# Optimization experiments

Hardware: AMD Instinct MI355X
Metric: run time of the kernel (lower is better)

The kernel has to match this reference:

```python
import jax, jax.numpy as jnp
import numpy as np

CHANNELS = 512
NUM_HEADS = 8
NUM_GROUPS = 32
EPS = 1e-5


def setup_inputs() -> dict:
    key = jax.random.key(0)
    ks = jax.random.split(key, 6)
    c = CHANNELS
    x = jax.random.normal(ks[0], (8, c, 32, 32), dtype=jnp.float32)
    norm_w = jnp.ones((c,), jnp.float32)
    norm_b = jnp.zeros((c,), jnp.float32)
    # 1x1 conv1d weights stored as [out, in]
    qkv_w = jax.random.normal(ks[1], (3 * c, c), jnp.float32) * (1.0 / np.sqrt(c))
    qkv_b = jax.random.normal(ks[2], (3 * c,), jnp.float32) * 0.02
    # proj_out is zero-initialized in the original; use small random values so the
    # residual branch is exercised numerically (init values are not part of the math).
    proj_w = jax.random.normal(ks[3], (c, c), jnp.float32) * 0.02
    proj_b = jax.random.normal(ks[4], (c,), jnp.float32) * 0.02
    return {"x": x, "norm_w": norm_w, "norm_b": norm_b,
            "qkv_w": qkv_w, "qkv_b": qkv_b, "proj_w": proj_w, "proj_b": proj_b}


def _group_norm(x, w, b):
    # x: [B, C, L]; normalize per (batch, group) over (C/G, L) in float32
    B, C, L = x.shape
    xg = x.astype(jnp.float32).reshape(B, NUM_GROUPS, (C // NUM_GROUPS) * L)
    mean = xg.mean(axis=-1, keepdims=True)
    var = xg.var(axis=-1, keepdims=True)
    xn = ((xg - mean) * jax.lax.rsqrt(var + EPS)).reshape(B, C, L)
    return (xn * w[None, :, None] + b[None, :, None]).astype(x.dtype)


def _attention_legacy(qkv, n_heads):
    # qkv: [B, 3*C, L]  (QKVAttentionLegacy: split heads after reshape)
    B, width, L = qkv.shape
    ch = width // (3 * n_heads)
    q, k, v = jnp.split(qkv.reshape(B * n_heads, 3 * ch, L), 3, axis=1)
    scale = 1.0 / np.sqrt(np.sqrt(ch))
    w = jnp.einsum('bct,bcs->bts', q * scale, k * scale)  # [B*H, L, L]
    w = jax.nn.softmax(w.astype(jnp.float32), axis=-1).astype(qkv.dtype)
    a = jnp.einsum('bts,bcs->bct', w, v)  # [B*H, ch, L]
    return a.reshape(B, n_heads * ch, L)


def reference(x, norm_w, norm_b, qkv_w, qkv_b, proj_w, proj_b):
    b, c = x.shape[0], x.shape[1]
    spatial = x.shape[2:]
    x_ = x.reshape(b, c, -1)  # [B, C, L]
    xn = _group_norm(x_, norm_w, norm_b)
    qkv = jnp.einsum('oc,bcl->bol', qkv_w, xn) + qkv_b[None, :, None]
    h = _attention_legacy(qkv, NUM_HEADS)
    h = jnp.einsum('oc,bcl->bol', proj_w, h) + proj_b[None, :, None]
    return (x_ + h).reshape(b, c, *spatial)
```

## Files before the change

kernel.cpp:

```cpp
#include <hip/hip_runtime.h>
#include <hip/hip_bf16.h>
#include <stdint.h>


#define NB 8
#define NC 512
#define NL 1024
#define NHD 8
#define ND 64

typedef __attribute__((ext_vector_type(4))) float f32x4;
typedef __attribute__((ext_vector_type(8))) short bf16x8;
typedef __attribute__((ext_vector_type(4))) short bf16x4;
typedef __attribute__((ext_vector_type(4))) unsigned short u16x4;
typedef __attribute__((ext_vector_type(8))) unsigned short u16x8;

#define MFMA16(a, b, c) __builtin_amdgcn_mfma_f32_16x16x32_bf16((a), (b), (c), 0, 0, 0)

static __device__ __forceinline__ f32x4 mfma_k16(bf16x4 a, bf16x4 b, f32x4 c) {
#if __has_builtin(__builtin_amdgcn_mfma_f32_16x16x16bf16_1k)
  return __builtin_amdgcn_mfma_f32_16x16x16bf16_1k(a, b, c, 0, 0, 0);
#else
  asm("v_mfma_f32_16x16x16_bf16 %0, %1, %2, %0" : "+v"(c) : "v"(a), "v"(b));
  return c;
#endif
}

#if __has_builtin(__builtin_amdgcn_exp2f)
#define EXP2F __builtin_amdgcn_exp2f
#else
#define EXP2F exp2f
#endif

static __device__ __forceinline__ unsigned short f2bf(float f) {
  union { float f; uint32_t u; } v; v.f = f;
  uint32_t r = v.u + 0x7fffu + ((v.u >> 16) & 1u);
  return (unsigned short)(r >> 16);
}

static __device__ __forceinline__ short f2bf_h(float f) {
  __hip_bfloat16 h = __float2bfloat16(f);
  return *reinterpret_cast<short*>(&h);
}

static __device__ __forceinline__ void gl_lds16(const unsigned short* g, unsigned short* l) {
  __builtin_amdgcn_global_load_lds(
      (const __attribute__((address_space(1))) void*)g,
      (__attribute__((address_space(3))) void*)l, 16, 0, 0);
}

__global__ __launch_bounds__(256) void k_conv_w(const float* __restrict__ qkvw,
                                                const float* __restrict__ pw,
                                                unsigned short* __restrict__ qwb,
                                                unsigned short* __restrict__ pwb) {
  int i = blockIdx.x * 256 + threadIdx.x;
  const int NQ4 = (3 * NC * NC) / 4;
  if (i < NQ4) {
    f32x4 v = ((const f32x4*)qkvw)[i];
    u16x4 o; o.x = f2bf(v.x); o.y = f2bf(v.y); o.z = f2bf(v.z); o.w = f2bf(v.w);
    ((u16x4*)qwb)[i] = o;
  } else {
    int j = i - NQ4;
    f32x4 v = ((const f32x4*)pw)[j];
    u16x4 o; o.x = f2bf(v.x); o.y = f2bf(v.y); o.z = f2bf(v.z); o.w = f2bf(v.w);
    ((u16x4*)pwb)[j] = o;
  }
}

__global__ __launch_bounds__(256) void k_gnorm(const float* __restrict__ x,
                                               const float* __restrict__ nw,
                                               const float* __restrict__ nb,
                                               unsigned short* __restrict__ xnt) {
  const int b = blockIdx.x >> 5, g = blockIdx.x & 31;
  const float* base = x + ((size_t)b * NC + g * 16) * NL;
  const int t = threadIdx.x;
  f32x4 vals[16];
  float s = 0.f, ss = 0.f;
#pragma unroll
  for (int r = 0; r < 16; ++r) {
    f32x4 v = ((const f32x4*)base)[t + 256 * r];
    vals[r] = v;
    s += v.x + v.y + v.z + v.w;
    ss += v.x * v.x + v.y * v.y + v.z * v.z + v.w * v.w;
  }
#pragma unroll
  for (int m = 1; m < 64; m <<= 1) { s += __shfl_xor(s, m, 64); ss += __shfl_xor(ss, m, 64); }
  __shared__ float red[8];
  const int w = t >> 6;
  if ((t & 63) == 0) { red[w] = s; red[4 + w] = ss; }
  __syncthreads();
  s  = red[0] + red[1] + red[2] + red[3];
  ss = red[4] + red[5] + red[6] + red[7];
  const float mean = s * (1.f / 16384.f);
  const float var  = ss * (1.f / 16384.f) - mean * mean;
  const float inv  = rsqrtf(var + 1e-5f);
  u16x8 ov[4][2];
#pragma unroll
  for (int r = 0; r < 16; ++r) {
    float wcv = nw[g * 16 + r] * inv;
    float bcv = nb[g * 16 + r] - mean * wcv;
    f32x4 v = vals[r];
    ov[0][r >> 3][r & 7] = f2bf(v.x * wcv + bcv);
    ov[1][r >> 3][r & 7] = f2bf(v.y * wcv + bcv);
    ov[2][r >> 3][r & 7] = f2bf(v.z * wcv + bcv);
    ov[3][r >> 3][r & 7] = f2bf(v.w * wcv + bcv);
  }
#pragma unroll
  for (int j = 0; j < 4; ++j) {
    size_t off = ((size_t)b * NL + 4 * t + j) * NC + g * 16;
    *(u16x8*)(xnt + off)     = ov[j][0];
    *(u16x8*)(xnt + off + 8) = ov[j][1];
  }
}

__global__ __launch_bounds__(256) void k_qkv(const unsigned short* __restrict__ xnt,
                                             const unsigned short* __restrict__ qwb,
                                             const float* __restrict__ qkvb,
                                             unsigned short* __restrict__ qt,
                                             unsigned short* __restrict__ kt,
                                             unsigned short* __restrict__ vt) {
  __shared__ __align__(16) unsigned short As[128 * 64];
  __shared__ __align__(16) unsigned short Bs[128 * 64];
  const int m0 = blockIdx.x * 128;
  const int n0 = blockIdx.y * 128;
  const int b = blockIdx.z;
  const int tid = threadIdx.x, lane = tid & 63, w = tid >> 6;
  const int wr = w >> 1, wc = w & 1;

  int soff[4];
#pragma unroll
  for (int r = 0; r < 4; ++r) {
    int c = (r * 4 + w) * 64 + lane;
    int row = c >> 3, lc = (c & 7) ^ (row & 7);
    soff[r] = row * NC + lc * 8;
  }
  const unsigned short* Ap = xnt + (size_t)b * NL * NC + (size_t)m0 * NC;
  const unsigned short* Bp = qwb + (size_t)n0 * NC;

  f32x4 acc[4][4];
#pragma unroll
  for (int mi = 0; mi < 4; ++mi)
#pragma unroll
    for (int ni = 0; ni < 4; ++ni) acc[mi][ni] = (f32x4){0.f, 0.f, 0.f, 0.f};

  for (int k0 = 0; k0 < NC; k0 += 64) {
#pragma unroll
    for (int r = 0; r < 4; ++r) gl_lds16(Ap + soff[r], &As[(r * 4 + w) * 512]);
#pragma unroll
    for (int r = 0; r < 4; ++r) gl_lds16(Bp + soff[r], &Bs[(r * 4 + w) * 512]);
    Ap += 64; Bp += 64;
    __syncthreads();
#pragma unroll
    for (int ks = 0; ks < 2; ++ks) {
      bf16x8 af[4], bfr[4];
#pragma unroll
      for (int mi = 0; mi < 4; ++mi) {
        int row = wr * 64 + mi * 16 + (lane & 15);
        int ph = ((lane >> 4) + ks * 4) ^ (row & 7);
        af[mi] = *(const bf16x8*)&As[row * 64 + ph * 8];
      }
#pragma unroll
      for (int ni = 0; ni < 4; ++ni) {
        int row = wc * 64 + ni * 16 + (lane & 15);
        int ph = ((lane >> 4) + ks * 4) ^ (row & 7);
        bfr[ni] = *(const bf16x8*)&Bs[row * 64 + ph * 8];
      }
#pragma unroll
      for (int mi = 0; mi < 4; ++mi)
#pragma unroll
        for (int ni = 0; ni < 4; ++ni)
          acc[mi][ni] = MFMA16(af[mi], bfr[ni], acc[mi][ni]);
    }
    __syncthreads();
  }
#pragma unroll
  for (int ni = 0; ni < 4; ++ni) {
    int o = n0 + wc * 64 + ni * 16 + (lane & 15);
    int head = o / 192, rem = o - head * 192;
    int type = rem >> 6, ch = rem & 63;
    float bias = qkvb[o];
#pragma unroll
    for (int mi = 0; mi < 4; ++mi) {
      int l0 = m0 + wr * 64 + mi * 16 + ((lane >> 4) << 2);
      if (type == 2) {
        u16x4 pk;
#pragma unroll
        for (int i = 0; i < 4; ++i) pk[i] = f2bf(acc[mi][ni][i] + bias);
        *(u16x4*)&vt[(((size_t)(b * NHD + head) * 256 + (l0 >> 2)) * ND + ch) * 4] = pk;
      } else {
        const float sc = (type == 0)
            ? (0.35355339059327373f * 1.4426950408889634f)
            : 0.35355339059327373f;
        unsigned short* dst =
            (type == 0 ? qt : kt) + ((size_t)(b * NHD + head) * NL + l0) * ND + ch;
#pragma unroll
        for (int i = 0; i < 4; ++i)
          dst[i * ND] = f2bf((acc[mi][ni][i] + bias) * sc);
      }
    }
  }
}

__global__ __launch_bounds__(256) void k_attn(const unsigned short* __restrict__ qt,
                                              const unsigned short* __restrict__ kt,
                                              const unsigned short* __restrict__ vt,
                                              unsigned short* __restrict__ abuf) {
  __shared__ __align__(16) unsigned short Ks[2][64 * 64];
  __shared__ __align__(16) unsigned short Vs[2][64 * 64];
  const int bid = blockIdx.x;
  const int bh = (bid & 7) * 8 + (bid >> 6);
  const int tb = (bid >> 3) & 7;
  const int tid = threadIdx.x, lane = tid & 63, w = tid >> 6;
  const int lo = lane & 15, g = lane >> 4;
  const int t0 = tb * 128 + w * 32;
  const unsigned short* qb = qt + (size_t)bh * NL * ND;

  int koff[2], voff[2];
#pragma unroll
  for (int r = 0; r < 2; ++r) {
    int c = (r * 4 + w) * 64 + lane;
    int row = c >> 3, lc = (c & 7) ^ (row & 7);
    koff[r] = row * ND + lc * 8;
    voff[r] = c * 8;
  }
  const int e0 = lo * 64 + ((g ^ (lo & 7)) * 8);
  const int e1 = lo * 64 + (((4 + g) ^ (lo & 7)) * 8);
  const int vbase = g * 256 + lo * 4;

  const unsigned short* kst = kt + (size_t)bh * NL * ND;
  const unsigned short* vst = vt + (size_t)bh * NL * ND;

  bf16x8 qf[2][2];
#pragma unroll
  for (int h = 0; h < 2; ++h)
#pragma unroll
    for (int ks = 0; ks < 2; ++ks)
      qf[h][ks] = *(const bf16x8*)&qb[(size_t)(t0 + h * 16 + lo) * ND + ks * 32 + g * 8];

  f32x4 pv[2][4];
#pragma unroll
  for (int h = 0; h < 2; ++h)
#pragma unroll
    for (int ci = 0; ci < 4; ++ci) pv[h][ci] = (f32x4){0.f, 0.f, 0.f, 0.f};
  float lsum0 = 0.f, lsum1 = 0.f;

  gl_lds16(kst + koff[0], &Ks[0][w * 512]);
  gl_lds16(kst + koff[1], &Ks[0][(4 + w) * 512]);
  gl_lds16(vst + voff[0], &Vs[0][w * 512]);
  gl_lds16(vst + voff[1], &Vs[0][(4 + w) * 512]);
  kst += 4096; vst += 4096;

#define ATTN_TILE(BUF, LAST)                                                  \
  {                                                                           \
    __syncthreads();                                                          \
    if (!(LAST)) {                                                            \
      gl_lds16(kst + koff[0], &Ks[(BUF) ^ 1][w * 512]);                       \
      gl_lds16(kst + koff[1], &Ks[(BUF) ^ 1][(4 + w) * 512]);                 \
      gl_lds16(vst + voff[0], &Vs[(BUF) ^ 1][w * 512]);                       \
      gl_lds16(vst + voff[1], &Vs[(BUF) ^ 1][(4 + w) * 512]);                 \
      kst += 4096; vst += 4096;                                               \
    }                                                                         \
    f32x4 sacc[2][4];                                                         \
    _Pragma("unroll")                                                         \
    for (int h = 0; h < 2; ++h)                                               \
      _Pragma("unroll")                                                       \
      for (int sblk = 0; sblk < 4; ++sblk)                                    \
        sacc[h][sblk] = (f32x4){0.f, 0.f, 0.f, 0.f};                          \
    __builtin_amdgcn_s_setprio(1);                                            \
    _Pragma("unroll")                                                         \
    for (int sblk = 0; sblk < 4; ++sblk) {                                    \
      bf16x8 kf = *(const bf16x8*)&Ks[BUF][sblk * 1024 + e0];                 \
      sacc[0][sblk] = MFMA16(kf, qf[0][0], sacc[0][sblk]);                    \
      sacc[1][sblk] = MFMA16(kf, qf[1][0], sacc[1][sblk]);                    \
    }                                                                         \
    _Pragma("unroll")                                                         \
    for (int sblk = 0; sblk < 4; ++sblk) {                                    \
      bf16x8 kf = *(const bf16x8*)&Ks[BUF][sblk * 1024 + e1];                 \
      sacc[0][sblk] = MFMA16(kf, qf[0][1], sacc[0][sblk]);                    \
      sacc[1][sblk] = MFMA16(kf, qf[1][1], sacc[1][sblk]);                    \
    }                                                                         \
    __builtin_amdgcn_s_setprio(0);                                            \
    _Pragma("unroll")                                                         \
    for (int sblk = 0; sblk < 4; ++sblk) {                                    \
      float a0 = EXP2F(fminf(sacc[0][sblk][0], 80.f));                        \
      float a1 = EXP2F(fminf(sacc[0][sblk][1], 80.f));                        \
      float a2 = EXP2F(fminf(sacc[0][sblk][2], 80.f));                        \
      float a3 = EXP2F(fminf(sacc[0][sblk][3], 80.f));                        \
      lsum0 += (a0 + a1) + (a2 + a3);                                         \
      bf16x4 pf0;                                                             \
      pf0[0] = f2bf_h(a0); pf0[1] = f2bf_h(a1);                               \
      pf0[2] = f2bf_h(a2); pf0[3] = f2bf_h(a3);                               \
      float b0 = EXP2F(fminf(sacc[1][sblk][0], 80.f));                        \
      float b1 = EXP2F(fminf(sacc[1][sblk][1], 80.f));                        \
      float b2 = EXP2F(fminf(sacc[1][sblk][2], 80.f));                        \
      float b3 = EXP2F(fminf(sacc[1][sblk][3], 80.f));                        \
      lsum1 += (b0 + b1) + (b2 + b3);                                         \
      bf16x4 pf1;                                                             \
      pf1[0] = f2bf_h(b0); pf1[1] = f2bf_h(b1);                               \
      pf1[2] = f2bf_h(b2); pf1[3] = f2bf_h(b3);                               \
      _Pragma("unroll")                                                       \
      for (int ci = 0; ci < 4; ++ci) {                                        \
        bf16x4 vf = *(const bf16x4*)&Vs[BUF][sblk * 1024 + ci * 64 + vbase];  \
        pv[0][ci] = mfma_k16(pf0, vf, pv[0][ci]);                             \
        pv[1][ci] = mfma_k16(pf1, vf, pv[1][ci]);                             \
      }                                                                       \
    }                                                                         \
  }

  for (int it = 0; it < 16; it += 2) {
    ATTN_TILE(0, false);
    ATTN_TILE(1, it == 14);
  }
#undef ATTN_TILE

#pragma unroll
  for (int h = 0; h < 2; ++h) {
    float l = h ? lsum1 : lsum0;
    l += __shfl_xor(l, 16);
    l += __shfl_xor(l, 32);
    float li[4];
#pragma unroll
    for (int i = 0; i < 4; ++i) li[i] = 1.0f / __shfl(l, g * 4 + i, 16);
#pragma unroll
    for (int ci = 0; ci < 4; ++ci)
#pragma unroll
      for (int i = 0; i < 4; ++i) {
        int tl = t0 + h * 16 + g * 4 + i;
        abuf[((size_t)bh * NL + tl) * ND + ci * 16 + lo] = f2bf_h(pv[h][ci][i] * li[i]);
      }
  }
}

__global__ __launch_bounds__(256) void k_proj(const unsigned short* __restrict__ abuf,
                                              const unsigned short* __restrict__ pwb,
                                              const float* __restrict__ pb,
                                              const float* __restrict__ x,
                                              float* __restrict__ out) {
  __shared__ __align__(16) unsigned short As[64 * 64];
  __shared__ __align__(16) unsigned short Bs[128 * 64];
  const int m0 = blockIdx.x * 64;
  const int n0 = blockIdx.y * 128;
  const int b = blockIdx.z;
  const int tid = threadIdx.x, lane = tid & 63, w = tid >> 6;
  const int lo = lane & 15, g = lane >> 4;

  int aoff[2], boff[4];
#pragma unroll
  for (int r = 0; r < 4; ++r) {
    int c = (r * 4 + w) * 64 + lane;
    int row = c >> 3, lc = (c & 7) ^ (row & 7);
    boff[r] = row * ND + lc * 8;
    if (r < 2) aoff[r] = row * NC + lc * 8;
  }
  const unsigned short* Ap = pwb + (size_t)m0 * NC;
  const unsigned short* Bp = abuf + ((size_t)(b * NHD) * NL + n0) * ND;

  f32x4 acc[4][2];
#pragma unroll
  for (int mi = 0; mi < 4; ++mi)
#pragma unroll
    for (int ni = 0; ni < 2; ++ni) acc[mi][ni] = (f32x4){0.f, 0.f, 0.f, 0.f};

  for (int k0 = 0; k0 < NC; k0 += 64) {
#pragma unroll
    for (int r = 0; r < 2; ++r) gl_lds16(Ap + aoff[r], &As[(r * 4 + w) * 512]);
#pragma unroll
    for (int r = 0; r < 4; ++r) gl_lds16(Bp + boff[r], &Bs[(r * 4 + w) * 512]);
    Ap += 64; Bp += (size_t)NL * ND;
    __syncthreads();
#pragma unroll
    for (int ks = 0; ks < 2; ++ks) {
      bf16x8 af[4], bfr[2];
#pragma unroll
      for (int mi = 0; mi < 4; ++mi) {
        int row = mi * 16 + lo;
        int ph = (g + ks * 4) ^ (row & 7);
        af[mi] = *(const bf16x8*)&As[row * 64 + ph * 8];
      }
#pragma unroll
      for (int ni = 0; ni < 2; ++ni) {
        int row = w * 32 + ni * 16 + lo;
        int ph = (g + ks * 4) ^ (row & 7);
        bfr[ni] = *(const bf16x8*)&Bs[row * 64 + ph * 8];
      }
#pragma unroll
      for (int mi = 0; mi < 4; ++mi)
#pragma unroll
        for (int ni = 0; ni < 2; ++ni)
          acc[mi][ni] = MFMA16(af[mi], bfr[ni], acc[mi][ni]);
    }
    __syncthreads();
  }
#pragma unroll
  for (int mi = 0; mi < 4; ++mi)
#pragma unroll
    for (int i = 0; i < 4; ++i) {
      int o = m0 + mi * 16 + g * 4 + i;
      float pbv = pb[o];
#pragma unroll
      for (int ni = 0; ni < 2; ++ni) {
        int l = n0 + w * 32 + ni * 16 + lo;
        size_t idx = ((size_t)b * NC + o) * NL + l;
        out[idx] = x[idx] + acc[mi][ni][i] + pbv;
      }
    }
}

extern "C" void kernel_launch(void* const* d_in, const int* in_sizes, int n_in,
                              void* d_out, int out_size, void* d_ws, size_t ws_size,
                              hipStream_t stream) {
  const float* x    = (const float*)d_in[0];
  const float* nw   = (const float*)d_in[1];
  const float* nb   = (const float*)d_in[2];
  const float* qkvw = (const float*)d_in[3];
  const float* qkvb = (const float*)d_in[4];
  const float* pw   = (const float*)d_in[5];
  const float* pb   = (const float*)d_in[6];
  float* out = (float*)d_out;

  char* ws = (char*)d_ws;
  unsigned short* xnt  = (unsigned short*)(ws);
  unsigned short* abuf = (unsigned short*)(ws);
  unsigned short* qwb  = (unsigned short*)(ws + 8388608);
  unsigned short* pwb  = (unsigned short*)(ws + 9961472);
  unsigned short* qt   = (unsigned short*)(ws + 10485760);
  unsigned short* kt   = (unsigned short*)(ws + 18874368);
  unsigned short* vt   = (unsigned short*)(ws + 27262976);

  k_conv_w<<<1024, 256, 0, stream>>>(qkvw, pw, qwb, pwb);
  k_gnorm<<<256, 256, 0, stream>>>(x, nw, nb, xnt);
  k_qkv<<<dim3(8, 12, 8), 256, 0, stream>>>(xnt, qwb, qkvb, qt, kt, vt);
  k_attn<<<512, 256, 0, stream>>>(qt, kt, vt, abuf);
  k_proj<<<dim3(8, 8, 8), 256, 0, stream>>>(abuf, pwb, pb, x, out);
}
```

Baseline: 92.96 us.

## Merge prep kernels, compute softmax row sums via MFMA, enlarge proj tile

Folds the weight-to-bf16 conversion and group norm into a single launch, which removes one kernel launch and its boundary. In attention, the per-row exp sums are now produced by an extra MFMA against a ones vector rather than VALU adds plus cross-lane shuffles, and the PV MFMAs are issued under raised wave priority. The projection GEMM tile grows from 64x128 to 128x128 with a 2x2 wave layout, halving the grid and giving more reuse per block. The risks are extra MFMA work and higher register pressure, and the row sums are now accumulated from bf16-rounded probabilities.

```diff
diff --git a/kernel.cpp b/kernel.cpp
--- a/kernel.cpp
+++ b/kernel.cpp
@@ -49,28 +49,29 @@
       (__attribute__((address_space(3))) void*)l, 16, 0, 0);
 }
 
-__global__ __launch_bounds__(256) void k_conv_w(const float* __restrict__ qkvw,
-                                                const float* __restrict__ pw,
-                                                unsigned short* __restrict__ qwb,
-                                                unsigned short* __restrict__ pwb) {
-  int i = blockIdx.x * 256 + threadIdx.x;
-  const int NQ4 = (3 * NC * NC) / 4;
-  if (i < NQ4) {
-    f32x4 v = ((const f32x4*)qkvw)[i];
-    u16x4 o; o.x = f2bf(v.x); o.y = f2bf(v.y); o.z = f2bf(v.z); o.w = f2bf(v.w);
-    ((u16x4*)qwb)[i] = o;
-  } else {
-    int j = i - NQ4;
-    f32x4 v = ((const f32x4*)pw)[j];
-    u16x4 o; o.x = f2bf(v.x); o.y = f2bf(v.y); o.z = f2bf(v.z); o.w = f2bf(v.w);
-    ((u16x4*)pwb)[j] = o;
-  }
-}
-
-__global__ __launch_bounds__(256) void k_gnorm(const float* __restrict__ x,
-                                               const float* __restrict__ nw,
-                                               const float* __restrict__ nb,
-                                               unsigned short* __restrict__ xnt) {
+__global__ __launch_bounds__(256) void k_pre(const float* __restrict__ x,
+                                             const float* __restrict__ nw,
+                                             const float* __restrict__ nb,
+                                             const float* __restrict__ qkvw,
+                                             const float* __restrict__ pw,
+                                             unsigned short* __restrict__ xnt,
+                                             unsigned short* __restrict__ qwb,
+                                             unsigned short* __restrict__ pwb) {
+  if (blockIdx.x >= 256) {
+    int i = (blockIdx.x - 256) * 256 + threadIdx.x;
+    const int NQ4 = (3 * NC * NC) / 4;
+    if (i < NQ4) {
+      f32x4 v = ((const f32x4*)qkvw)[i];
+      u16x4 o; o.x = f2bf(v.x); o.y = f2bf(v.y); o.z = f2bf(v.z); o.w = f2bf(v.w);
+      ((u16x4*)qwb)[i] = o;
+    } else {
+      int j = i - NQ4;
+      f32x4 v = ((const f32x4*)pw)[j];
+      u16x4 o; o.x = f2bf(v.x); o.y = f2bf(v.y); o.z = f2bf(v.z); o.w = f2bf(v.w);
+      ((u16x4*)pwb)[j] = o;
+    }
+    return;
+  }
   const int b = blockIdx.x >> 5, g = blockIdx.x & 31;
   const float* base = x + ((size_t)b * NC + g * 16) * NL;
   const int t = threadIdx.x;
@@ -237,12 +238,18 @@
     for (int ks = 0; ks < 2; ++ks)
       qf[h][ks] = *(const bf16x8*)&qb[(size_t)(t0 + h * 16 + lo) * ND + ks * 32 + g * 8];
 
+  bf16x4 vones;
+#pragma unroll
+  for (int j = 0; j < 4; ++j) vones[j] = (short)0x3F80;
+
   f32x4 pv[2][4];
 #pragma unroll
   for (int h = 0; h < 2; ++h)
 #pragma unroll
     for (int ci = 0; ci < 4; ++ci) pv[h][ci] = (f32x4){0.f, 0.f, 0.f, 0.f};
-  float lsum0 = 0.f, lsum1 = 0.f;
+  f32x4 lacc[2];
+  lacc[0] = (f32x4){0.f, 0.f, 0.f, 0.f};
+  lacc[1] = (f32x4){0.f, 0.f, 0.f, 0.f};
 
   gl_lds16(kst + koff[0], &Ks[0][w * 512]);
   gl_lds16(kst + koff[1], &Ks[0][(4 + w) * 512]);
@@ -286,7 +293,6 @@
       float a1 = EXP2F(fminf(sacc[0][sblk][1], 80.f));                        \
       float a2 = EXP2F(fminf(sacc[0][sblk][2], 80.f));                        \
       float a3 = EXP2F(fminf(sacc[0][sblk][3], 80.f));                        \
-      lsum0 += (a0 + a1) + (a2 + a3);                                         \
       bf16x4 pf0;                                                             \
       pf0[0] = f2bf_h(a0); pf0[1] = f2bf_h(a1);                               \
       pf0[2] = f2bf_h(a2); pf0[3] = f2bf_h(a3);                               \
@@ -294,16 +300,19 @@
       float b1 = EXP2F(fminf(sacc[1][sblk][1], 80.f));                        \
       float b2 = EXP2F(fminf(sacc[1][sblk][2], 80.f));                        \
       float b3 = EXP2F(fminf(sacc[1][sblk][3], 80.f));                        \
-      lsum1 += (b0 + b1) + (b2 + b3);                                         \
       bf16x4 pf1;                                                             \
       pf1[0] = f2bf_h(b0); pf1[1] = f2bf_h(b1);                               \
       pf1[2] = f2bf_h(b2); pf1[3] = f2bf_h(b3);                               \
+      __builtin_amdgcn_s_setprio(1);                                          \
+      lacc[0] = mfma_k16(pf0, vones, lacc[0]);                                \
+      lacc[1] = mfma_k16(pf1, vones, lacc[1]);                                \
       _Pragma("unroll")                                                       \
       for (int ci = 0; ci < 4; ++ci) {                                        \
         bf16x4 vf = *(const bf16x4*)&Vs[BUF][sblk * 1024 + ci * 64 + vbase];  \
         pv[0][ci] = mfma_k16(pf0, vf, pv[0][ci]);                             \
         pv[1][ci] = mfma_k16(pf1, vf, pv[1][ci]);                             \
       }                                                                       \
+      __builtin_amdgcn_s_setprio(0);                                          \
     }                                                                         \
   }
 
@@ -315,12 +324,9 @@
 
 #pragma unroll
   for (int h = 0; h < 2; ++h) {
-    float l = h ? lsum1 : lsum0;
-    l += __shfl_xor(l, 16);
-    l += __shfl_xor(l, 32);
     float li[4];
 #pragma unroll
-    for (int i = 0; i < 4; ++i) li[i] = 1.0f / __shfl(l, g * 4 + i, 16);
+    for (int i = 0; i < 4; ++i) li[i] = 1.0f / lacc[h][i];
 #pragma unroll
     for (int ci = 0; ci < 4; ++ci)
 #pragma unroll
@@ -336,57 +342,57 @@
                                               const float* __restrict__ pb,
                                               const float* __restrict__ x,
                                               float* __restrict__ out) {
-  __shared__ __align__(16) unsigned short As[64 * 64];
+  __shared__ __align__(16) unsigned short As[128 * 64];
   __shared__ __align__(16) unsigned short Bs[128 * 64];
-  const int m0 = blockIdx.x * 64;
+  const int m0 = blockIdx.x * 128;
   const int n0 = blockIdx.y * 128;
   const int b = blockIdx.z;
   const int tid = threadIdx.x, lane = tid & 63, w = tid >> 6;
-  const int lo = lane & 15, g = lane >> 4;
-
-  int aoff[2], boff[4];
+  const int wr = w >> 1, wc = w & 1;
+
+  int aoff[4], boff[4];
 #pragma unroll
   for (int r = 0; r < 4; ++r) {
     int c = (r * 4 + w) * 64 + lane;
     int row = c >> 3, lc = (c & 7) ^ (row & 7);
+    aoff[r] = row * NC + lc * 8;
     boff[r] = row * ND + lc * 8;
-    if (r < 2) aoff[r] = row * NC + lc * 8;
   }
   const unsigned short* Ap = pwb + (size_t)m0 * NC;
   const unsigned short* Bp = abuf + ((size_t)(b * NHD) * NL + n0) * ND;
 
-  f32x4 acc[4][2];
+  f32x4 acc[4][4];
 #pragma unroll
   for (int mi = 0; mi < 4; ++mi)
 #pragma unroll
-    for (int ni = 0; ni < 2; ++ni) acc[mi][ni] = (f32x4){0.f, 0.f, 0.f, 0.f};
+    for (int ni = 0; ni < 4; ++ni) acc[mi][ni] = (f32x4){0.f, 0.f, 0.f, 0.f};
 
   for (int k0 = 0; k0 < NC; k0 += 64) {
 #pragma unroll
-    for (int r = 0; r < 2; ++r) gl_lds16(Ap + aoff[r], &As[(r * 4 + w) * 512]);
+    for (int r = 0; r < 4; ++r) gl_lds16(Ap + aoff[r], &As[(r * 4 + w) * 512]);
 #pragma unroll
     for (int r = 0; r < 4; ++r) gl_lds16(Bp + boff[r], &Bs[(r * 4 + w) * 512]);
     Ap += 64; Bp += (size_t)NL * ND;
     __syncthreads();
 #pragma unroll
     for (int ks = 0; ks < 2; ++ks) {
-      bf16x8 af[4], bfr[2];
+      bf16x8 af[4], bfr[4];
 #pragma unroll
       for (int mi = 0; mi < 4; ++mi) {
-        int row = mi * 16 + lo;
-        int ph = (g + ks * 4) ^ (row & 7);
+        int row = wr * 64 + mi * 16 + (lane & 15);
+        int ph = ((lane >> 4) + ks * 4) ^ (row & 7);
         af[mi] = *(const bf16x8*)&As[row * 64 + ph * 8];
       }
 #pragma unroll
-      for (int ni = 0; ni < 2; ++ni) {
-        int row = w * 32 + ni * 16 + lo;
-        int ph = (g + ks * 4) ^ (row & 7);
+      for (int ni = 0; ni < 4; ++ni) {
+        int row = wc * 64 + ni * 16 + (lane & 15);
+        int ph = ((lane >> 4) + ks * 4) ^ (row & 7);
         bfr[ni] = *(const bf16x8*)&Bs[row * 64 + ph * 8];
       }
 #pragma unroll
       for (int mi = 0; mi < 4; ++mi)
 #pragma unroll
-        for (int ni = 0; ni < 2; ++ni)
+        for (int ni = 0; ni < 4; ++ni)
           acc[mi][ni] = MFMA16(af[mi], bfr[ni], acc[mi][ni]);
     }
     __syncthreads();
@@ -395,11 +401,11 @@
   for (int mi = 0; mi < 4; ++mi)
 #pragma unroll
     for (int i = 0; i < 4; ++i) {
-      int o = m0 + mi * 16 + g * 4 + i;
+      int o = m0 + wr * 64 + mi * 16 + ((lane >> 4) << 2) + i;
       float pbv = pb[o];
 #pragma unroll
-      for (int ni = 0; ni < 2; ++ni) {
-        int l = n0 + w * 32 + ni * 16 + lo;
+      for (int ni = 0; ni < 4; ++ni) {
+        int l = n0 + wc * 64 + ni * 16 + (lane & 15);
         size_t idx = ((size_t)b * NC + o) * NL + l;
         out[idx] = x[idx] + acc[mi][ni][i] + pbv;
       }
@@ -427,9 +433,8 @@
   unsigned short* kt   = (unsigned short*)(ws + 18874368);
   unsigned short* vt   = (unsigned short*)(ws + 27262976);
 
-  k_conv_w<<<1024, 256, 0, stream>>>(qkvw, pw, qwb, pwb);
-  k_gnorm<<<256, 256, 0, stream>>>(x, nw, nb, xnt);
+  k_pre<<<1280, 256, 0, stream>>>(x, nw, nb, qkvw, pw, xnt, qwb, pwb);
   k_qkv<<<dim3(8, 12, 8), 256, 0, stream>>>(xnt, qwb, qkvb, qt, kt, vt);
   k_attn<<<512, 256, 0, stream>>>(qt, kt, vt, abuf);
-  k_proj<<<dim3(8, 8, 8), 256, 0, stream>>>(abuf, pwb, pb, x, out);
-}
+  k_proj<<<dim3(4, 8, 8), 256, 0, stream>>>(abuf, pwb, pb, x, out);
+}
```

New measurement: 83.66 us. -10.0%, faster.
